# Performance work log

Measured on AMD Instinct MI355X. Metric: run time of the kernel, lower is better.

## Reference

```python
import jax, jax.numpy as jnp
import numpy as np

N, K, IN_DIM, OUT_DIM = 131072, 16, 256, 128


def setup_inputs() -> dict:
    key = jax.random.key(0)
    ks = jax.random.split(key, 6)
    s1 = 1.0 / np.sqrt(IN_DIM)
    s2 = 1.0 / np.sqrt(OUT_DIM)
    return {
        "x": jax.random.normal(ks[0], (N, IN_DIM), dtype=jnp.float32),
        "z": jax.random.randint(ks[1], (N,), 0, K, dtype=jnp.int32),
        "W1": jax.random.uniform(ks[2], (K, IN_DIM, OUT_DIM), jnp.float32, -s1, s1),
        "b1": jax.random.uniform(ks[3], (K, OUT_DIM), jnp.float32, -s1, s1),
        "W2": jax.random.uniform(ks[4], (K, OUT_DIM, 2), jnp.float32, -s2, s2),
        "b2": jax.random.uniform(ks[5], (K, 2), jnp.float32, -s2, s2),
    }


def reference(x, z, W1, b1, W2, b2):
    # Per-cluster expert MLP: tokens with z==i go through expert i.
    # Loop over the fixed, small number of experts (k); data dims stay vectorized.
    k = W1.shape[0]
    ri = jnp.zeros((x.shape[0], 2), dtype=x.dtype)
    for i in range(k):
        h = jax.nn.relu(x @ W1[i] + b1[i])          # [N, out_dim]
        logits = h @ W2[i] + b2[i]                  # [N, 2]
        ri = jnp.where((z == i)[:, None], logits, ri)
    # Every z in [0, k) is covered, so every row of ri has been written
    # (matches the torch path where non-empty clusters overwrite -inf).
    return jax.nn.softmax(ri, axis=-1)
```

## Files before the change

kernel.cpp:

```cpp
#include <hip/hip_runtime.h>
#include <hip/hip_bf16.h>

#define KEXP   16
#define IN_DIM 256
#define OUT_DIM 128
#define TILE   128

typedef float f32x4 __attribute__((ext_vector_type(4)));
typedef short bf16x8 __attribute__((ext_vector_type(8)));

__device__ __forceinline__ short f2bf(float f) {
    union { float f; unsigned u; } v; v.f = f;
    return (short)((v.u + 0x7fffu + ((v.u >> 16) & 1u)) >> 16);
}

__global__ __launch_bounds__(256) void prep_k(const float* __restrict__ W1,
                                              ushort* __restrict__ w1t,
                                              const int* __restrict__ z,
                                              int* __restrict__ counts, int n) {
    __shared__ float ld[64][65];
    int bid = blockIdx.x, tid = threadIdx.x;
    if (bid < 128) {
        int e = bid >> 3, sub = bid & 7;
        int k0 = (sub & 3) * 64, n0 = (sub >> 2) * 64;
        const float* src = W1 + (long)e * (IN_DIM * OUT_DIM);
        int tr = tid >> 6, tc = tid & 63;
#pragma unroll
        for (int i = 0; i < 16; i++) {
            int row = i * 4 + tr;
            ld[row][tc] = src[(k0 + row) * OUT_DIM + n0 + tc];
        }
        __syncthreads();
        ushort* dst = w1t + (long)e * (OUT_DIM * IN_DIM);
#pragma unroll
        for (int i = 0; i < 16; i++) {
            int nrow = i * 4 + tr;
            dst[(n0 + nrow) * IN_DIM + k0 + tc] = (ushort)f2bf(ld[tc][nrow]);
        }
    } else {
        int* h = (int*)ld;
        if (tid < KEXP) h[tid] = 0;
        __syncthreads();
        for (int i = (bid - 128) * 256 + tid; i < n; i += 256 * 256)
            atomicAdd(&h[z[i]], 1);
        __syncthreads();
        if (tid < KEXP) atomicAdd(&counts[tid], h[tid]);
    }
}

__global__ void scan_k(const int* __restrict__ counts, int* __restrict__ bases,
                       int* __restrict__ tb) {
    if (threadIdx.x == 0) {
        int acc = 0, tacc = 0;
        for (int i = 0; i < KEXP; i++) {
            bases[i] = acc;
            tb[i] = tacc;
            acc += counts[i];
            tacc += (counts[i] + TILE - 1) / TILE;
        }
        tb[KEXP] = tacc;
    }
}

__global__ __launch_bounds__(256) void scatter_k(const int* __restrict__ z,
                                                 const int* __restrict__ bases,
                                                 int* __restrict__ cursors,
                                                 int* __restrict__ perm, int n) {
    __shared__ int lc[KEXP];
    __shared__ int lb[KEXP];
    int tid = threadIdx.x;
    if (tid < KEXP) lc[tid] = 0;
    __syncthreads();
    int i = blockIdx.x * 256 + tid;
    int e = 0, r = 0;
    if (i < n) {
        e = z[i];
        r = atomicAdd(&lc[e], 1);
    }
    __syncthreads();
    if (tid < KEXP && lc[tid] > 0) lb[tid] = atomicAdd(&cursors[tid], lc[tid]);
    __syncthreads();
    if (i < n) perm[bases[e] + lb[e] + r] = i;
}

__global__ __launch_bounds__(256) void mlp_k(
    const float* __restrict__ x, const float* __restrict__ b1,
    const float* __restrict__ W2, const float* __restrict__ b2,
    const int* __restrict__ counts, const int* __restrict__ bases,
    const int* __restrict__ tb, const int* __restrict__ perm,
    const ushort* __restrict__ w1t, float* __restrict__ out) {
    __shared__ char smem[65536];
    int b = blockIdx.x;
    if (b >= tb[KEXP]) return;
    int e = 0;
#pragma unroll
    for (int i = 1; i < KEXP; i++)
        if (b >= tb[i]) e = i;
    int t = b - tb[e];
    int nrem = counts[e] - t * TILE;
    int pbase = bases[e] + t * TILE;

    int tid = threadIdx.x;
    int lane = tid & 63, wid = tid >> 6;
    int li = lane & 15, q = lane >> 4;

    int m0 = wid * 32 + li;
    int m1 = wid * 32 + 16 + li;
    int g0 = perm[pbase + (m0 < nrem ? m0 : 0)];
    int g1 = perm[pbase + (m1 < nrem ? m1 : 0)];
    const float* xr0 = x + (long)g0 * IN_DIM;
    const float* xr1 = x + (long)g1 * IN_DIM;

    f32x4 a0[8][2], a1[8][2];
#pragma unroll
    for (int kk = 0; kk < 8; kk++) {
        int k0 = kk * 32 + q * 8;
        a0[kk][0] = *(const f32x4*)(xr0 + k0);
        a0[kk][1] = *(const f32x4*)(xr0 + k0 + 4);
        a1[kk][0] = *(const f32x4*)(xr1 + k0);
        a1[kk][1] = *(const f32x4*)(xr1 + k0 + 4);
    }

    const char* wsrc = (const char*)(w1t + (long)e * (OUT_DIM * IN_DIM));
#pragma unroll
    for (int it = 0; it < 16; it++) {
        int byte = (it * 256 + tid) * 16;
        uint4 v = *(const uint4*)(wsrc + byte);
        int row = byte >> 9;
        *(uint4*)(smem + (byte ^ ((row & 7) << 4))) = v;
    }
    __syncthreads();

    bf16x8 af0[8], af1[8];
#pragma unroll
    for (int kk = 0; kk < 8; kk++) {
#pragma unroll
        for (int j = 0; j < 4; j++) {
            af0[kk][j]     = f2bf(a0[kk][0][j]);
            af0[kk][j + 4] = f2bf(a0[kk][1][j]);
            af1[kk][j]     = f2bf(a1[kk][0][j]);
            af1[kk][j + 4] = f2bf(a1[kk][1][j]);
        }
    }

    f32x4 acc0[8], acc1[8];
#pragma unroll
    for (int n = 0; n < 8; n++) { acc0[n] = (f32x4)0.0f; acc1[n] = (f32x4)0.0f; }

#pragma unroll
    for (int kk = 0; kk < 8; kk++) {
#pragma unroll
        for (int n = 0; n < 8; n++) {
            int col = n * 16 + li;
            int byte = col * 512 + kk * 64 + q * 16;
            bf16x8 bf = *(const bf16x8*)(smem + (byte ^ ((col & 7) << 4)));
            acc0[n] = __builtin_amdgcn_mfma_f32_16x16x32_bf16(af0[kk], bf, acc0[n], 0, 0, 0);
            acc1[n] = __builtin_amdgcn_mfma_f32_16x16x32_bf16(af1[kk], bf, acc1[n], 0, 0, 0);
        }
    }

    float p[2][2][4];
#pragma unroll
    for (int mt = 0; mt < 2; mt++)
#pragma unroll
        for (int l = 0; l < 2; l++)
#pragma unroll
            for (int r = 0; r < 4; r++) p[mt][l][r] = 0.0f;

#pragma unroll
    for (int n = 0; n < 8; n++) {
        int col = n * 16 + li;
        float bb = b1[e * OUT_DIM + col];
        float w0 = W2[e * OUT_DIM * 2 + col * 2 + 0];
        float w1 = W2[e * OUT_DIM * 2 + col * 2 + 1];
#pragma unroll
        for (int r = 0; r < 4; r++) {
            float h0 = fmaxf(acc0[n][r] + bb, 0.0f);
            float h1 = fmaxf(acc1[n][r] + bb, 0.0f);
            p[0][0][r] += h0 * w0;
            p[0][1][r] += h0 * w1;
            p[1][0][r] += h1 * w0;
            p[1][1][r] += h1 * w1;
        }
    }
#pragma unroll
    for (int m = 1; m < 16; m <<= 1)
#pragma unroll
        for (int mt = 0; mt < 2; mt++)
#pragma unroll
            for (int l = 0; l < 2; l++)
#pragma unroll
                for (int r = 0; r < 4; r++)
                    p[mt][l][r] += __shfl_xor(p[mt][l][r], m, 64);

    if (li == 0) {
        float bb0 = b2[e * 2], bb1 = b2[e * 2 + 1];
#pragma unroll
        for (int mt = 0; mt < 2; mt++)
#pragma unroll
            for (int r = 0; r < 4; r++) {
                int mm = wid * 32 + mt * 16 + q * 4 + r;
                if (mm < nrem) {
                    int orig = perm[pbase + mm];
                    float l0 = p[mt][0][r] + bb0, l1 = p[mt][1][r] + bb1;
                    float mx = fmaxf(l0, l1);
                    float e0 = __expf(l0 - mx), e1 = __expf(l1 - mx);
                    float inv = 1.0f / (e0 + e1);
                    *(float2*)(out + (long)orig * 2) = make_float2(e0 * inv, e1 * inv);
                }
            }
    }
}

extern "C" void kernel_launch(void* const* d_in, const int* in_sizes, int n_in,
                              void* d_out, int out_size, void* d_ws, size_t ws_size,
                              hipStream_t stream) {
    const float* x  = (const float*)d_in[0];
    const int*   z  = (const int*)d_in[1];
    const float* W1 = (const float*)d_in[2];
    const float* b1 = (const float*)d_in[3];
    const float* W2 = (const float*)d_in[4];
    const float* b2 = (const float*)d_in[5];
    float* out = (float*)d_out;
    int n = in_sizes[1];

    int* counts  = (int*)d_ws;
    int* cursors = counts + 16;
    int* basesp  = counts + 32;
    int* tbp     = counts + 48;
    int* perm    = counts + 256;
    ushort* w1t  = (ushort*)((char*)d_ws + 1024 + (size_t)n * 4);

    hipMemsetAsync(counts, 0, 128, stream);
    prep_k<<<384, 256, 0, stream>>>(W1, w1t, z, counts, n);
    scan_k<<<1, 64, 0, stream>>>(counts, basesp, tbp);
    scatter_k<<<(n + 255) / 256, 256, 0, stream>>>(z, basesp, cursors, perm, n);

    int maxtiles = (n + TILE - 1) / TILE + (KEXP - 1);
    mlp_k<<<maxtiles, 256, 0, stream>>>(x, b1, W2, b2, counts, basesp, tbp, perm, w1t, out);
}
```

Before: 252.1 us.

## Make MLP kernel persistent per expert with LDS-resident weights and x prefetch

```diff
diff --git a/kernel.cpp b/kernel.cpp
--- a/kernel.cpp
+++ b/kernel.cpp
@@ -5,13 +5,16 @@
 #define IN_DIM 256
 #define OUT_DIM 128
 #define TILE   128
+#define BPE    16
 
 typedef float f32x4 __attribute__((ext_vector_type(4)));
 typedef short bf16x8 __attribute__((ext_vector_type(8)));
-
-__device__ __forceinline__ short f2bf(float f) {
+typedef const unsigned int __attribute__((address_space(1)))* gptr_t;
+typedef unsigned int __attribute__((address_space(3)))* lptr_t;
+
+__device__ __forceinline__ ushort f2bf(float f) {
     union { float f; unsigned u; } v; v.f = f;
-    return (short)((v.u + 0x7fffu + ((v.u >> 16) & 1u)) >> 16);
+    return (ushort)((v.u + 0x7fffu + ((v.u >> 16) & 1u)) >> 16);
 }
 
 __global__ __launch_bounds__(256) void prep_k(const float* __restrict__ W1,
@@ -31,11 +34,13 @@
             ld[row][tc] = src[(k0 + row) * OUT_DIM + n0 + tc];
         }
         __syncthreads();
-        ushort* dst = w1t + (long)e * (OUT_DIM * IN_DIM);
-#pragma unroll
-        for (int i = 0; i < 16; i++) {
-            int nrow = i * 4 + tr;
-            dst[(n0 + nrow) * IN_DIM + k0 + tc] = (ushort)f2bf(ld[tc][nrow]);
+        char* dst = (char*)w1t + (long)e * (OUT_DIM * IN_DIM * 2);
+#pragma unroll
+        for (int i = 0; i < 16; i++) {
+            int col = n0 + i * 4 + tr;
+            int L = (col * IN_DIM + k0 + tc) * 2;
+            int S = L ^ ((col & 7) << 4);
+            *(ushort*)(dst + S) = f2bf(ld[tc][i * 4 + tr]);
         }
     } else {
         int* h = (int*)ld;
@@ -48,17 +53,10 @@
     }
 }
 
-__global__ void scan_k(const int* __restrict__ counts, int* __restrict__ bases,
-                       int* __restrict__ tb) {
+__global__ void scan_k(const int* __restrict__ counts, int* __restrict__ bases) {
     if (threadIdx.x == 0) {
-        int acc = 0, tacc = 0;
-        for (int i = 0; i < KEXP; i++) {
-            bases[i] = acc;
-            tb[i] = tacc;
-            acc += counts[i];
-            tacc += (counts[i] + TILE - 1) / TILE;
-        }
-        tb[KEXP] = tacc;
+        int acc = 0;
+        for (int i = 0; i < KEXP; i++) { bases[i] = acc; acc += counts[i]; }
     }
 }
 
@@ -83,132 +81,133 @@
     if (i < n) perm[bases[e] + lb[e] + r] = i;
 }
 
-__global__ __launch_bounds__(256) void mlp_k(
+__global__ __launch_bounds__(512, 2) void mlp_k(
     const float* __restrict__ x, const float* __restrict__ b1,
     const float* __restrict__ W2, const float* __restrict__ b2,
     const int* __restrict__ counts, const int* __restrict__ bases,
-    const int* __restrict__ tb, const int* __restrict__ perm,
-    const ushort* __restrict__ w1t, float* __restrict__ out) {
-    __shared__ char smem[65536];
+    const int* __restrict__ perm, const ushort* __restrict__ w1t,
+    float* __restrict__ out) {
+    __shared__ char Wl[65536];
+    __shared__ char Al[65536];
+
     int b = blockIdx.x;
-    if (b >= tb[KEXP]) return;
-    int e = 0;
-#pragma unroll
-    for (int i = 1; i < KEXP; i++)
-        if (b >= tb[i]) e = i;
-    int t = b - tb[e];
-    int nrem = counts[e] - t * TILE;
-    int pbase = bases[e] + t * TILE;
+    int e = b >> 4, slot = b & 15;
+    int cnt = counts[e];
+    int pb0 = bases[e];
+    int ntiles = (cnt + TILE - 1) / TILE;
 
     int tid = threadIdx.x;
-    int lane = tid & 63, wid = tid >> 6;
+    int lane = tid & 63, w = tid >> 6;
     int li = lane & 15, q = lane >> 4;
 
-    int m0 = wid * 32 + li;
-    int m1 = wid * 32 + 16 + li;
-    int g0 = perm[pbase + (m0 < nrem ? m0 : 0)];
-    int g1 = perm[pbase + (m1 < nrem ? m1 : 0)];
-    const float* xr0 = x + (long)g0 * IN_DIM;
-    const float* xr1 = x + (long)g1 * IN_DIM;
-
-    f32x4 a0[8][2], a1[8][2];
-#pragma unroll
-    for (int kk = 0; kk < 8; kk++) {
-        int k0 = kk * 32 + q * 8;
-        a0[kk][0] = *(const f32x4*)(xr0 + k0);
-        a0[kk][1] = *(const f32x4*)(xr0 + k0 + 4);
-        a1[kk][0] = *(const f32x4*)(xr1 + k0);
-        a1[kk][1] = *(const f32x4*)(xr1 + k0 + 4);
-    }
-
-    const char* wsrc = (const char*)(w1t + (long)e * (OUT_DIM * IN_DIM));
-#pragma unroll
-    for (int it = 0; it < 16; it++) {
-        int byte = (it * 256 + tid) * 16;
-        uint4 v = *(const uint4*)(wsrc + byte);
-        int row = byte >> 9;
-        *(uint4*)(smem + (byte ^ ((row & 7) << 4))) = v;
-    }
-    __syncthreads();
-
-    bf16x8 af0[8], af1[8];
-#pragma unroll
-    for (int kk = 0; kk < 8; kk++) {
-#pragma unroll
-        for (int j = 0; j < 4; j++) {
-            af0[kk][j]     = f2bf(a0[kk][0][j]);
-            af0[kk][j + 4] = f2bf(a0[kk][1][j]);
-            af1[kk][j]     = f2bf(a1[kk][0][j]);
-            af1[kk][j + 4] = f2bf(a1[kk][1][j]);
-        }
-    }
-
-    f32x4 acc0[8], acc1[8];
-#pragma unroll
-    for (int n = 0; n < 8; n++) { acc0[n] = (f32x4)0.0f; acc1[n] = (f32x4)0.0f; }
-
-#pragma unroll
-    for (int kk = 0; kk < 8; kk++) {
-#pragma unroll
-        for (int n = 0; n < 8; n++) {
-            int col = n * 16 + li;
-            int byte = col * 512 + kk * 64 + q * 16;
-            bf16x8 bf = *(const bf16x8*)(smem + (byte ^ ((col & 7) << 4)));
-            acc0[n] = __builtin_amdgcn_mfma_f32_16x16x32_bf16(af0[kk], bf, acc0[n], 0, 0, 0);
-            acc1[n] = __builtin_amdgcn_mfma_f32_16x16x32_bf16(af1[kk], bf, acc1[n], 0, 0, 0);
-        }
-    }
-
-    float p[2][2][4];
-#pragma unroll
-    for (int mt = 0; mt < 2; mt++)
-#pragma unroll
-        for (int l = 0; l < 2; l++)
-#pragma unroll
-            for (int r = 0; r < 4; r++) p[mt][l][r] = 0.0f;
-
-#pragma unroll
-    for (int n = 0; n < 8; n++) {
-        int col = n * 16 + li;
-        float bb = b1[e * OUT_DIM + col];
-        float w0 = W2[e * OUT_DIM * 2 + col * 2 + 0];
-        float w1 = W2[e * OUT_DIM * 2 + col * 2 + 1];
-#pragma unroll
-        for (int r = 0; r < 4; r++) {
-            float h0 = fmaxf(acc0[n][r] + bb, 0.0f);
-            float h1 = fmaxf(acc1[n][r] + bb, 0.0f);
-            p[0][0][r] += h0 * w0;
-            p[0][1][r] += h0 * w1;
-            p[1][0][r] += h1 * w0;
-            p[1][1][r] += h1 * w1;
-        }
-    }
-#pragma unroll
-    for (int m = 1; m < 16; m <<= 1)
-#pragma unroll
-        for (int mt = 0; mt < 2; mt++)
-#pragma unroll
-            for (int l = 0; l < 2; l++)
-#pragma unroll
-                for (int r = 0; r < 4; r++)
-                    p[mt][l][r] += __shfl_xor(p[mt][l][r], m, 64);
-
-    if (li == 0) {
-        float bb0 = b2[e * 2], bb1 = b2[e * 2 + 1];
-#pragma unroll
-        for (int mt = 0; mt < 2; mt++)
+    const char* wsrc = (const char*)w1t + (long)e * (OUT_DIM * IN_DIM * 2);
+#pragma unroll
+    for (int i = 0; i < 8; i++) {
+        int off = w * 8192 + i * 1024;
+        __builtin_amdgcn_global_load_lds((gptr_t)(wsrc + off + lane * 16),
+                                         (lptr_t)(Wl + off), 16, 0, 0);
+    }
+
+    float bbv[8], w2a[8], w2b[8];
+#pragma unroll
+    for (int nn = 0; nn < 8; nn++) {
+        int col = nn * 16 + li;
+        bbv[nn] = b1[e * OUT_DIM + col];
+        w2a[nn] = W2[(e * OUT_DIM + col) * 2 + 0];
+        w2b[nn] = W2[(e * OUT_DIM + col) * 2 + 1];
+    }
+    float bb0 = b2[e * 2 + 0], bb1 = b2[e * 2 + 1];
+
+    f32x4 av[16];
+    int pb_cur = 0, nr_cur = 0;
+    if (slot < ntiles) {
+        pb_cur = pb0 + slot * TILE;
+        nr_cur = cnt - slot * TILE;
+        int rr = w * 16 + li;
+        int pv = perm[pb_cur + (rr < nr_cur ? rr : nr_cur - 1)];
+#pragma unroll
+        for (int i = 0; i < 16; i++) {
+            int g = __shfl(pv, i, 16);
+            av[i] = *(const f32x4*)((const char*)x + (long)g * 1024 + lane * 16);
+        }
+    }
+
+    for (int t = slot; t < ntiles; t += BPE) {
+#pragma unroll
+        for (int i = 0; i < 16; i++) {
+            int r = w * 16 + i;
+            uint2 pk;
+            pk.x = (unsigned)f2bf(av[i][0]) | ((unsigned)f2bf(av[i][1]) << 16);
+            pk.y = (unsigned)f2bf(av[i][2]) | ((unsigned)f2bf(av[i][3]) << 16);
+            *(uint2*)(Al + r * 512 + ((lane * 8) ^ ((r & 7) << 4))) = pk;
+        }
+        __syncthreads();
+
+        int tn = t + BPE;
+        int pb_nx = 0, nr_nx = 0;
+        if (tn < ntiles) {
+            pb_nx = pb0 + tn * TILE;
+            nr_nx = cnt - tn * TILE;
+            int rr = w * 16 + li;
+            int pv = perm[pb_nx + (rr < nr_nx ? rr : nr_nx - 1)];
+#pragma unroll
+            for (int i = 0; i < 16; i++) {
+                int g = __shfl(pv, i, 16);
+                av[i] = *(const f32x4*)((const char*)x + (long)g * 1024 + lane * 16);
+            }
+        }
+
+        f32x4 acc[8];
+#pragma unroll
+        for (int nn = 0; nn < 8; nn++) acc[nn] = (f32x4)0.0f;
+
+        int arow = w * 16 + li;
+        int aswz = (arow & 7) << 4;
+#pragma unroll
+        for (int kk = 0; kk < 8; kk++) {
+            bf16x8 af = *(const bf16x8*)(Al + arow * 512 + ((kk * 64 + q * 16) ^ aswz));
+#pragma unroll
+            for (int nn = 0; nn < 8; nn++) {
+                int col = nn * 16 + li;
+                bf16x8 bf = *(const bf16x8*)(Wl + col * 512 + ((kk * 64 + q * 16) ^ ((col & 7) << 4)));
+                acc[nn] = __builtin_amdgcn_mfma_f32_16x16x32_bf16(af, bf, acc[nn], 0, 0, 0);
+            }
+        }
+
+        float p0[4] = {0.f, 0.f, 0.f, 0.f}, p1[4] = {0.f, 0.f, 0.f, 0.f};
+#pragma unroll
+        for (int nn = 0; nn < 8; nn++) {
 #pragma unroll
             for (int r = 0; r < 4; r++) {
-                int mm = wid * 32 + mt * 16 + q * 4 + r;
-                if (mm < nrem) {
-                    int orig = perm[pbase + mm];
-                    float l0 = p[mt][0][r] + bb0, l1 = p[mt][1][r] + bb1;
+                float h = fmaxf(acc[nn][r] + bbv[nn], 0.0f);
+                p0[r] += h * w2a[nn];
+                p1[r] += h * w2b[nn];
+            }
+        }
+#pragma unroll
+        for (int m = 1; m < 16; m <<= 1)
+#pragma unroll
+            for (int r = 0; r < 4; r++) {
+                p0[r] += __shfl_xor(p0[r], m, 64);
+                p1[r] += __shfl_xor(p1[r], m, 64);
+            }
+        if (li == 0) {
+#pragma unroll
+            for (int r = 0; r < 4; r++) {
+                int mm = w * 16 + q * 4 + r;
+                if (mm < nr_cur) {
+                    int orig = perm[pb_cur + mm];
+                    float l0 = p0[r] + bb0, l1 = p1[r] + bb1;
                     float mx = fmaxf(l0, l1);
                     float e0 = __expf(l0 - mx), e1 = __expf(l1 - mx);
                     float inv = 1.0f / (e0 + e1);
                     *(float2*)(out + (long)orig * 2) = make_float2(e0 * inv, e1 * inv);
                 }
             }
+        }
+        __syncthreads();
+        pb_cur = pb_nx;
+        nr_cur = nr_nx;
     }
 }
 
@@ -227,15 +226,12 @@
     int* counts  = (int*)d_ws;
     int* cursors = counts + 16;
     int* basesp  = counts + 32;
-    int* tbp     = counts + 48;
     int* perm    = counts + 256;
     ushort* w1t  = (ushort*)((char*)d_ws + 1024 + (size_t)n * 4);
 
     hipMemsetAsync(counts, 0, 128, stream);
     prep_k<<<384, 256, 0, stream>>>(W1, w1t, z, counts, n);
-    scan_k<<<1, 64, 0, stream>>>(counts, basesp, tbp);
+    scan_k<<<1, 64, 0, stream>>>(counts, basesp);
     scatter_k<<<(n + 255) / 256, 256, 0, stream>>>(z, basesp, cursors, perm, n);
-
-    int maxtiles = (n + TILE - 1) / TILE + (KEXP - 1);
-    mlp_k<<<maxtiles, 256, 0, stream>>>(x, b1, W2, b2, counts, basesp, tbp, perm, w1t, out);
-}
+    mlp_k<<<KEXP * BPE, 512, 0, stream>>>(x, b1, W2, b2, counts, basesp, perm, w1t, out);
+}
```

Result: faster. 228.7 us (-9.3%).
